# Kernel tuning notes

Measured on AMD Instinct MI355X. Metric: run time of the kernel, lower is better.

Reference implementation:

```python
import jax, jax.numpy as jnp
import numpy as np

# Static configuration (matches init_kwargs / input_specs)
B = 4          # number of point clouds (equal-sized)
NPER = 4096    # points per cloud
RATIO = 0.25
MPER = int(NPER * RATIO)  # sampled centroids per cloud
R = 0.2        # ball-query radius
K = 64         # max_num_neighbors
C = 64         # feature dim


def setup_inputs() -> dict:
    key = jax.random.key(0)
    ks = jax.random.split(key, 6)
    N = B * NPER
    x = jax.random.normal(ks[0], (N, C), dtype=jnp.float32)
    pos = jax.random.uniform(ks[1], (N, 3), dtype=jnp.float32)
    batch = (jnp.arange(N) // NPER).astype(jnp.int64)
    weight = jax.random.normal(ks[2], (N,), dtype=jnp.float32)
    # local_nn = Seq(Lin(67,128), ReLU, Lin(128,256), ReLU)
    W1 = jax.random.normal(ks[3], (C + 3, 128), dtype=jnp.float32) / np.float32(np.sqrt(C + 3))
    b1 = jnp.zeros((128,), dtype=jnp.float32)
    W2 = jax.random.normal(ks[4], (128, 256), dtype=jnp.float32) / np.float32(np.sqrt(128))
    b2 = jnp.zeros((256,), dtype=jnp.float32)
    return {"x": x, "pos": pos, "batch": batch, "weight": weight,
            "W1": W1, "b1": b1, "W2": W2, "b2": b2}


def _fps_single(p):
    """Farthest point sampling on one cloud p:[NPER,3] -> MPER int32 indices.
    Deterministic start at index 0 (torch_geometric uses a random start)."""
    n = p.shape[0]
    def step(carry, _):
        mind, last = carry
        d = jnp.sum((p - p[last]) ** 2, axis=-1)
        mind = jnp.minimum(mind, d)
        nxt = jnp.argmax(mind).astype(jnp.int32)
        return (mind, nxt), last
    init = (jnp.full((n,), jnp.inf, dtype=p.dtype), jnp.int32(0))
    _, idx = jax.lax.scan(step, init, None, length=MPER)
    return idx  # [MPER]


def reference(x, pos, batch, weight, W1, b1, W2, b2):
    pos_b = pos.reshape(B, NPER, 3)
    x_b = x.reshape(B, NPER, C)

    # --- FPS per cloud (vectorized over clouds) ---
    idx = jax.vmap(_fps_single)(pos_b)                      # [B, MPER] local indices

    qpos = jnp.take_along_axis(pos_b, idx[:, :, None], axis=1)  # [B, MPER, 3]

    # --- radius ball query: K nearest within r (fixed-size, batch-respecting) ---
    d2 = jnp.sum((qpos[:, :, None, :] - pos_b[:, None, :, :]) ** 2, axis=-1)  # [B,MPER,NPER]
    neg, nbr = jax.lax.top_k(-d2, K)                        # [B, MPER, K]
    valid = (-neg) <= jnp.float32(R * R)                    # [B, MPER, K]

    # --- gather neighbor features / positions ---
    flat = nbr.reshape(B, MPER * K)
    x_j = jnp.take_along_axis(x_b, flat[:, :, None], axis=1).reshape(B, MPER, K, C)
    pos_j = jnp.take_along_axis(pos_b, flat[:, :, None], axis=1).reshape(B, MPER, K, 3)
    rel = pos_j - qpos[:, :, None, :]                       # [B, MPER, K, 3]

    # --- PointNetConv: local_nn(concat(x_j, rel)) then max aggregation ---
    msg = jnp.concatenate([x_j, rel], axis=-1)              # [B, MPER, K, C+3]
    h = jax.nn.relu(jnp.einsum('bmkc,cd->bmkd', msg, W1) + b1)
    h = jax.nn.relu(jnp.einsum('bmkd,de->bmke', h, W2) + b2)
    h = jnp.where(valid[:, :, :, None], h, -jnp.inf)
    x_out = jnp.max(h, axis=2).reshape(B * MPER, -1)        # [B*MPER, 256]

    # --- gather sampled pos / batch / weight using global indices ---
    idx_g = (idx + (jnp.arange(B, dtype=jnp.int32) * NPER)[:, None]).reshape(-1)
    pos_out = pos[idx_g]
    batch_out = batch[idx_g]
    weight_out = weight[idx_g]
    return x_out, pos_out, batch_out, weight_out
```

## Files before the change

### kernel.cpp

```cpp
#include <hip/hip_runtime.h>

#define NPER 4096
#define MPER 1024
#define KNB 64
#define NB 4

typedef __attribute__((ext_vector_type(8))) short short8_t;
typedef __attribute__((ext_vector_type(4))) float f32x4;
typedef __attribute__((ext_vector_type(2))) float f32x2;

__device__ __forceinline__ unsigned short f2bf(float f) {
  union { float f; unsigned u; } v; v.f = f;
  unsigned r = v.u + 0x7fffu + ((v.u >> 16) & 1u);
  return (unsigned short)(r >> 16);
}

__device__ __forceinline__ f32x2 pk_add(f32x2 a, f32x2 b) {
  f32x2 d; asm("v_pk_add_f32 %0, %1, %2" : "=v"(d) : "v"(a), "v"(b)); return d;
}
__device__ __forceinline__ f32x2 pk_mul(f32x2 a, f32x2 b) {
  f32x2 d; asm("v_pk_mul_f32 %0, %1, %2" : "=v"(d) : "v"(a), "v"(b)); return d;
}

#define DPP_KEY_STEP(ctrl)                                                            \
  {                                                                                   \
    unsigned lo = (unsigned)k, hi = (unsigned)(k >> 32);                              \
    unsigned tlo = (unsigned)__builtin_amdgcn_update_dpp((int)lo, (int)lo, ctrl, 0xF, 0xF, false); \
    unsigned thi = (unsigned)__builtin_amdgcn_update_dpp((int)hi, (int)hi, ctrl, 0xF, 0xF, false); \
    unsigned long long tk = ((unsigned long long)thi << 32) | tlo;                    \
    if (tk > k) k = tk;                                                               \
  }

#define U64MAX(a, b) (((a) > (b)) ? (a) : (b))

__global__ __launch_bounds__(256) void fps_kernel(const float* __restrict__ pos,
                                                  int* __restrict__ idxout) {
  __shared__ float4 p4[NPER];
  __shared__ alignas(16) unsigned long long candk[2][4];
  __shared__ int s_idx[MPER];
  const int b = blockIdx.x, t = threadIdx.x;
  const int wid = t >> 6, lane = t & 63;
  const int base = b * NPER;

  for (int i = t; i < NPER; i += 256) {
    p4[i] = make_float4(pos[(size_t)(base + i) * 3 + 0],
                        pos[(size_t)(base + i) * 3 + 1],
                        pos[(size_t)(base + i) * 3 + 2], 0.f);
  }
  __syncthreads();

  f32x2 pxp[8], pyp[8], pzp[8];
  float mnd[16];
  const int i0 = t * 16;
#pragma unroll
  for (int p = 0; p < 8; ++p) {
    float4 a = p4[i0 + 2 * p];
    float4 c = p4[i0 + 2 * p + 1];
    pxp[p] = (f32x2){a.x, c.x};
    pyp[p] = (f32x2){a.y, c.y};
    pzp[p] = (f32x2){a.z, c.z};
  }
#pragma unroll
  for (int j = 0; j < 16; ++j) mnd[j] = __builtin_inff();

  int last = 0;
  for (int it = 0; it < MPER; ++it) {
    if (t == 0) s_idx[it] = last;
    if (it == MPER - 1) break;
    const float4 q = p4[last];
    const f32x2 nqx = (f32x2){-q.x, -q.x};
    const f32x2 nqy = (f32x2){-q.y, -q.y};
    const f32x2 nqz = (f32x2){-q.z, -q.z};
    float bv = -1.0f; int bj = 0;
#pragma unroll
    for (int p = 0; p < 8; ++p) {
      f32x2 dx = pk_add(pxp[p], nqx);
      f32x2 dy = pk_add(pyp[p], nqy);
      f32x2 dz = pk_add(pzp[p], nqz);
      f32x2 s = pk_add(pk_add(pk_mul(dx, dx), pk_mul(dy, dy)), pk_mul(dz, dz));
      float m0 = fminf(mnd[2 * p], s.x);     mnd[2 * p] = m0;
      if (m0 > bv) { bv = m0; bj = 2 * p; }
      float m1 = fminf(mnd[2 * p + 1], s.y); mnd[2 * p + 1] = m1;
      if (m1 > bv) { bv = m1; bj = 2 * p + 1; }
    }
    const int bi = i0 + bj;
    union { float f; unsigned u; } fu; fu.f = bv;
    unsigned long long k = ((unsigned long long)fu.u << 32) | (0xFFFFFFFFu - (unsigned)bi);
    DPP_KEY_STEP(0x128)
    DPP_KEY_STEP(0x124)
    DPP_KEY_STEP(0x122)
    DPP_KEY_STEP(0x121)
    DPP_KEY_STEP(0x142)
    DPP_KEY_STEP(0x143)
    if (lane == 63) candk[it & 1][wid] = k;
    __syncthreads();
    const ulonglong2* ck = (const ulonglong2*)&candk[it & 1][0];
    ulonglong2 c0 = ck[0], c1 = ck[1];
    unsigned long long m0 = U64MAX(c0.x, c0.y);
    unsigned long long m1 = U64MAX(c1.x, c1.y);
    unsigned long long mg = U64MAX(m0, m1);
    last = (int)(0xFFFFFFFFu - (unsigned)mg);
  }
  __syncthreads();
  for (int i = t; i < MPER; i += 256) idxout[b * MPER + i] = s_idx[i];
}

#define CAP 1024
__global__ __launch_bounds__(256) void ballq_kernel(const float* __restrict__ pos,
                                                    const int* __restrict__ idx,
                                                    int* __restrict__ nbr) {
  __shared__ float cd[CAP];
  __shared__ int   ci[CAP];
  __shared__ int   s_cnt;
  const int c = blockIdx.x;
  const int b = c >> 10;
  const int t = threadIdx.x;
  const int base = b * NPER;
  if (t == 0) s_cnt = 0;
  __syncthreads();
  const int qi = idx[c];
  const float qx = pos[(size_t)(base + qi) * 3 + 0];
  const float qy = pos[(size_t)(base + qi) * 3 + 1];
  const float qz = pos[(size_t)(base + qi) * 3 + 2];
  const float r2f = (float)(0.2 * 0.2);
#pragma unroll
  for (int s = 0; s < 16; ++s) {
    const int i = t + s * 256;
    float dx = __fsub_rn(qx, pos[(size_t)(base + i) * 3 + 0]);
    float dy = __fsub_rn(qy, pos[(size_t)(base + i) * 3 + 1]);
    float dz = __fsub_rn(qz, pos[(size_t)(base + i) * 3 + 2]);
    float d = __fadd_rn(__fadd_rn(__fmul_rn(dx, dx), __fmul_rn(dy, dy)), __fmul_rn(dz, dz));
    if (d <= r2f) {
      int p = atomicAdd(&s_cnt, 1);
      if (p < CAP) { cd[p] = d; ci[p] = i; }
    }
  }
  __syncthreads();
  int n = s_cnt; if (n > CAP) n = CAP;
  if (n > KNB) {
    int P = 64; while (P < n) P <<= 1;
    for (int i = n + t; i < P; i += 256) { cd[i] = __builtin_inff(); ci[i] = 0x7fffffff; }
    __syncthreads();
    for (int k2 = 2; k2 <= P; k2 <<= 1) {
      for (int j = k2 >> 1; j > 0; j >>= 1) {
        for (int i = t; i < P; i += 256) {
          const int ixj = i ^ j;
          if (ixj > i) {
            const bool up = ((i & k2) == 0);
            float a = cd[i], bb = cd[ixj];
            int ia = ci[i], ib = ci[ixj];
            const bool gt = (a > bb) || (a == bb && ia > ib);
            if (gt == up) { cd[i] = bb; cd[ixj] = a; ci[i] = ib; ci[ixj] = ia; }
          }
        }
        __syncthreads();
      }
    }
  }
  if (t < KNB) nbr[c * KNB + t] = (t < n) ? ci[t] : -1;
}

__global__ __launch_bounds__(256) void prep_kernel(const float* __restrict__ W1,
                                                   const float* __restrict__ W2,
                                                   unsigned short* __restrict__ w1f,
                                                   unsigned short* __restrict__ w2f) {
  const int f = blockIdx.x * 256 + threadIdx.x;
  if (f < 12288) {
    const int frag = f >> 9, r = f & 511, lane = r >> 3, e = r & 7;
    const int nt = frag / 3, kt = frag % 3;
    const int n = nt * 16 + (lane & 15);
    const int k = kt * 32 + (lane >> 4) * 8 + e;
    float v = (k < 67) ? W1[k * 128 + n] : 0.f;
    w1f[f] = f2bf(v);
  } else if (f < 12288 + 32768) {
    const int g = f - 12288;
    const int frag = g >> 9, r = g & 511, lane = r >> 3, e = r & 7;
    const int nt = frag >> 2, kt = frag & 3;
    const int n = nt * 16 + (lane & 15);
    const int k = kt * 32 + (lane >> 4) * 8 + e;
    w2f[g] = f2bf(W2[k * 256 + n]);
  }
}

__global__ __launch_bounds__(256) void mlp_kernel(const float* __restrict__ x,
                                                  const float* __restrict__ pos,
                                                  const int* __restrict__ idx,
                                                  const int* __restrict__ nbr,
                                                  const unsigned short* __restrict__ w1f,
                                                  const unsigned short* __restrict__ w2f,
                                                  const float* __restrict__ b1,
                                                  const float* __restrict__ b2,
                                                  float* __restrict__ out) {
  __shared__ alignas(16) unsigned short s_msg[64][104];
  __shared__ alignas(16) unsigned short s_h1[64][136];
  __shared__ int   s_valid[64];
  __shared__ float s_red[4][256];

  const int c = blockIdx.x;
  const int b = c >> 10;
  const int t = threadIdx.x;
  const int wave = t >> 6, lane = t & 63;
  const int base = b * NPER;

  const int qi = idx[c];
  const float q0 = pos[(size_t)(base + qi) * 3 + 0];
  const float q1 = pos[(size_t)(base + qi) * 3 + 1];
  const float q2 = pos[(size_t)(base + qi) * 3 + 2];

  const int nbrv = nbr[c * KNB + lane];
  s_valid[lane] = (nbrv >= 0) ? 1 : 0;

#pragma unroll 4
  for (int i = 0; i < 16; ++i) {
    const int k = wave * 16 + i;
    const int j = __shfl(nbrv, k, 64);
    float f = 0.f;
    if (j >= 0) f = x[(size_t)(base + j) * 64 + lane];
    s_msg[k][lane] = f2bf(f);
    if (lane < 40) {
      float rv = 0.f;
      if (lane < 3 && j >= 0) {
        float p = pos[(size_t)(base + j) * 3 + lane];
        float qq = (lane == 0) ? q0 : ((lane == 1) ? q1 : q2);
        rv = __fsub_rn(p, qq);
      }
      s_msg[k][64 + lane] = f2bf(rv);
    }
  }
  __syncthreads();

  const int row = wave * 16 + (lane & 15);
  const int kofs = (lane >> 4) * 8;

  short8_t a1[3];
#pragma unroll
  for (int kt = 0; kt < 3; ++kt)
    a1[kt] = *(const short8_t*)&s_msg[row][kt * 32 + kofs];
  f32x4 acc1[8];
#pragma unroll
  for (int nt = 0; nt < 8; ++nt) acc1[nt] = (f32x4){0.f, 0.f, 0.f, 0.f};
#pragma unroll
  for (int kt = 0; kt < 3; ++kt) {
#pragma unroll
    for (int nt = 0; nt < 8; ++nt) {
      short8_t bf = *(const short8_t*)&w1f[((nt * 3 + kt) * 64 + lane) * 8];
      acc1[nt] = __builtin_amdgcn_mfma_f32_16x16x32_bf16(a1[kt], bf, acc1[nt], 0, 0, 0);
    }
  }
#pragma unroll
  for (int nt = 0; nt < 8; ++nt) {
    const int n = nt * 16 + (lane & 15);
    const float bias = b1[n];
    f32x4 v = acc1[nt];
#pragma unroll
    for (int e = 0; e < 4; ++e) {
      const int m = wave * 16 + (lane >> 4) * 4 + e;
      float h = v[e] + bias;
      h = (h > 0.f) ? h : 0.f;
      s_h1[m][n] = f2bf(h);
    }
  }
  __syncthreads();

  short8_t a2[4];
#pragma unroll
  for (int kt = 0; kt < 4; ++kt)
    a2[kt] = *(const short8_t*)&s_h1[row][kt * 32 + kofs];
  f32x4 acc2[16];
#pragma unroll
  for (int nt = 0; nt < 16; ++nt) acc2[nt] = (f32x4){0.f, 0.f, 0.f, 0.f};
#pragma unroll
  for (int kt = 0; kt < 4; ++kt) {
#pragma unroll
    for (int nt = 0; nt < 16; ++nt) {
      short8_t bf = *(const short8_t*)&w2f[((nt * 4 + kt) * 64 + lane) * 8];
      acc2[nt] = __builtin_amdgcn_mfma_f32_16x16x32_bf16(a2[kt], bf, acc2[nt], 0, 0, 0);
    }
  }
  const int m0 = wave * 16 + (lane >> 4) * 4;
  const int vld0 = s_valid[m0 + 0], vld1 = s_valid[m0 + 1];
  const int vld2 = s_valid[m0 + 2], vld3 = s_valid[m0 + 3];
#pragma unroll
  for (int nt = 0; nt < 16; ++nt) {
    const int n = nt * 16 + (lane & 15);
    const float bias = b2[n];
    f32x4 d = acc2[nt];
    float best = -__builtin_inff();
    {
      float h;
      h = d[0] + bias; h = (h > 0.f) ? h : 0.f; if (vld0) best = fmaxf(best, h);
      h = d[1] + bias; h = (h > 0.f) ? h : 0.f; if (vld1) best = fmaxf(best, h);
      h = d[2] + bias; h = (h > 0.f) ? h : 0.f; if (vld2) best = fmaxf(best, h);
      h = d[3] + bias; h = (h > 0.f) ? h : 0.f; if (vld3) best = fmaxf(best, h);
    }
    best = fmaxf(best, __shfl_xor(best, 16, 64));
    best = fmaxf(best, __shfl_xor(best, 32, 64));
    if ((lane >> 4) == 0) s_red[wave][n] = best;
  }
  __syncthreads();
  const float r = fmaxf(fmaxf(s_red[0][t], s_red[1][t]), fmaxf(s_red[2][t], s_red[3][t]));
  out[(size_t)c * 256 + t] = r;
}

__global__ __launch_bounds__(256) void tail_kernel(const float* __restrict__ pos,
                                                   const float* __restrict__ weight,
                                                   const int* __restrict__ idx,
                                                   float* __restrict__ out) {
  const int t = blockIdx.x * 256 + threadIdx.x;
  if (t >= NB * MPER) return;
  const int b = t >> 10;
  const int qi = idx[t];
  const int g = b * NPER + qi;
  float* pos_out = out + 1048576;
  float* batch_out = out + 1048576 + 12288;
  float* w_out = out + 1048576 + 12288 + 4096;
  pos_out[t * 3 + 0] = pos[(size_t)g * 3 + 0];
  pos_out[t * 3 + 1] = pos[(size_t)g * 3 + 1];
  pos_out[t * 3 + 2] = pos[(size_t)g * 3 + 2];
  batch_out[t] = (float)b;
  w_out[t] = weight[g];
}

extern "C" void kernel_launch(void* const* d_in, const int* in_sizes, int n_in,
                              void* d_out, int out_size, void* d_ws, size_t ws_size,
                              hipStream_t stream) {
  const float* x      = (const float*)d_in[0];
  const float* pos    = (const float*)d_in[1];
  const float* weight = (const float*)d_in[3];
  const float* W1     = (const float*)d_in[4];
  const float* b1     = (const float*)d_in[5];
  const float* W2     = (const float*)d_in[6];
  const float* b2     = (const float*)d_in[7];
  float* out = (float*)d_out;

  char* ws = (char*)d_ws;
  int* idx = (int*)ws;
  int* nbr = (int*)(ws + 16384);
  unsigned short* w1f = (unsigned short*)(ws + 16384 + 1048576);
  unsigned short* w2f = (unsigned short*)(ws + 16384 + 1048576 + 24576);

  prep_kernel<<<176, 256, 0, stream>>>(W1, W2, w1f, w2f);
  fps_kernel<<<NB, 256, 0, stream>>>(pos, idx);
  ballq_kernel<<<NB * MPER, 256, 0, stream>>>(pos, idx, nbr);
  mlp_kernel<<<NB * MPER, 256, 0, stream>>>(x, pos, idx, nbr, w1f, w2f, b1, b2, out);
  tail_kernel<<<16, 256, 0, stream>>>(pos, weight, idx, out);
}
```

Baseline: 782.8 us.

## Replace FPS barrier with tagged spin-wait and fuse ball query into MLP

The FPS loop drops its per-iteration __syncthreads. Each wave's candidate key now carries a 10-bit iteration tag and is published with a workgroup-scoped atomic store, and every wave spins until all four slots hold the current tag. The ball-query kernel is merged into the MLP kernel, so neighbor indices stay in shared memory and the global nbr round trip and one launch go away. The risks are spin-wait livelock or ordering hazards across the double-buffered slots, and higher LDS use per MLP block, which may reduce occupancy.

```diff
diff --git a/kernel.cpp b/kernel.cpp
--- a/kernel.cpp
+++ b/kernel.cpp
@@ -36,12 +36,13 @@
 __global__ __launch_bounds__(256) void fps_kernel(const float* __restrict__ pos,
                                                   int* __restrict__ idxout) {
   __shared__ float4 p4[NPER];
-  __shared__ alignas(16) unsigned long long candk[2][4];
+  __shared__ unsigned long long candk[2][4];
   __shared__ int s_idx[MPER];
   const int b = blockIdx.x, t = threadIdx.x;
   const int wid = t >> 6, lane = t & 63;
   const int base = b * NPER;
 
+  if (t < 8) ((unsigned long long*)candk)[t] = 1023ull;
   for (int i = t; i < NPER; i += 256) {
     p4[i] = make_float4(pos[(size_t)(base + i) * 3 + 0],
                         pos[(size_t)(base + i) * 3 + 1],
@@ -85,50 +86,97 @@
     }
     const int bi = i0 + bj;
     union { float f; unsigned u; } fu; fu.f = bv;
-    unsigned long long k = ((unsigned long long)fu.u << 32) | (0xFFFFFFFFu - (unsigned)bi);
+    const unsigned tg = (unsigned)it & 1023u;
+    unsigned long long k = ((unsigned long long)fu.u << 32) |
+                           ((unsigned long long)(4095u - (unsigned)bi) << 10) | tg;
     DPP_KEY_STEP(0x128)
     DPP_KEY_STEP(0x124)
     DPP_KEY_STEP(0x122)
     DPP_KEY_STEP(0x121)
     DPP_KEY_STEP(0x142)
     DPP_KEY_STEP(0x143)
-    if (lane == 63) candk[it & 1][wid] = k;
-    __syncthreads();
-    const ulonglong2* ck = (const ulonglong2*)&candk[it & 1][0];
-    ulonglong2 c0 = ck[0], c1 = ck[1];
-    unsigned long long m0 = U64MAX(c0.x, c0.y);
-    unsigned long long m1 = U64MAX(c1.x, c1.y);
-    unsigned long long mg = U64MAX(m0, m1);
-    last = (int)(0xFFFFFFFFu - (unsigned)mg);
+    const int s = it & 1;
+    if (lane == 63)
+      __hip_atomic_store(&candk[s][wid], k, __ATOMIC_RELAXED, __HIP_MEMORY_SCOPE_WORKGROUP);
+    unsigned long long k0, k1, k2, k3;
+    for (;;) {
+      k0 = __hip_atomic_load(&candk[s][0], __ATOMIC_RELAXED, __HIP_MEMORY_SCOPE_WORKGROUP);
+      k1 = __hip_atomic_load(&candk[s][1], __ATOMIC_RELAXED, __HIP_MEMORY_SCOPE_WORKGROUP);
+      k2 = __hip_atomic_load(&candk[s][2], __ATOMIC_RELAXED, __HIP_MEMORY_SCOPE_WORKGROUP);
+      k3 = __hip_atomic_load(&candk[s][3], __ATOMIC_RELAXED, __HIP_MEMORY_SCOPE_WORKGROUP);
+      unsigned m = (((unsigned)k0 & 1023u) ^ tg) | (((unsigned)k1 & 1023u) ^ tg) |
+                   (((unsigned)k2 & 1023u) ^ tg) | (((unsigned)k3 & 1023u) ^ tg);
+      if (m == 0) break;
+    }
+    unsigned long long ma = U64MAX(k0, k1);
+    unsigned long long mb = U64MAX(k2, k3);
+    unsigned long long mg = U64MAX(ma, mb);
+    last = 4095 - (int)((mg >> 10) & 0xFFFu);
   }
   __syncthreads();
   for (int i = t; i < MPER; i += 256) idxout[b * MPER + i] = s_idx[i];
 }
 
+__global__ __launch_bounds__(256) void prep_kernel(const float* __restrict__ W1,
+                                                   const float* __restrict__ W2,
+                                                   unsigned short* __restrict__ w1f,
+                                                   unsigned short* __restrict__ w2f) {
+  const int f = blockIdx.x * 256 + threadIdx.x;
+  if (f < 12288) {
+    const int frag = f >> 9, r = f & 511, lane = r >> 3, e = r & 7;
+    const int nt = frag / 3, kt = frag % 3;
+    const int n = nt * 16 + (lane & 15);
+    const int k = kt * 32 + (lane >> 4) * 8 + e;
+    float v = (k < 67) ? W1[k * 128 + n] : 0.f;
+    w1f[f] = f2bf(v);
+  } else if (f < 12288 + 32768) {
+    const int g = f - 12288;
+    const int frag = g >> 9, r = g & 511, lane = r >> 3, e = r & 7;
+    const int nt = frag >> 2, kt = frag & 3;
+    const int n = nt * 16 + (lane & 15);
+    const int k = kt * 32 + (lane >> 4) * 8 + e;
+    w2f[g] = f2bf(W2[k * 256 + n]);
+  }
+}
+
 #define CAP 1024
-__global__ __launch_bounds__(256) void ballq_kernel(const float* __restrict__ pos,
-                                                    const int* __restrict__ idx,
-                                                    int* __restrict__ nbr) {
+__global__ __launch_bounds__(256) void mlp_kernel(const float* __restrict__ x,
+                                                  const float* __restrict__ pos,
+                                                  const int* __restrict__ idx,
+                                                  const unsigned short* __restrict__ w1f,
+                                                  const unsigned short* __restrict__ w2f,
+                                                  const float* __restrict__ b1,
+                                                  const float* __restrict__ b2,
+                                                  float* __restrict__ out) {
   __shared__ float cd[CAP];
   __shared__ int   ci[CAP];
   __shared__ int   s_cnt;
+  __shared__ alignas(16) unsigned short s_msg[64][104];
+  __shared__ alignas(16) unsigned short s_h1[64][136];
+  __shared__ int   s_valid[64];
+  __shared__ float s_red[4][256];
+
   const int c = blockIdx.x;
   const int b = c >> 10;
   const int t = threadIdx.x;
+  const int wave = t >> 6, lane = t & 63;
   const int base = b * NPER;
+
   if (t == 0) s_cnt = 0;
   __syncthreads();
+
   const int qi = idx[c];
-  const float qx = pos[(size_t)(base + qi) * 3 + 0];
-  const float qy = pos[(size_t)(base + qi) * 3 + 1];
-  const float qz = pos[(size_t)(base + qi) * 3 + 2];
+  const float q0 = pos[(size_t)(base + qi) * 3 + 0];
+  const float q1 = pos[(size_t)(base + qi) * 3 + 1];
+  const float q2 = pos[(size_t)(base + qi) * 3 + 2];
   const float r2f = (float)(0.2 * 0.2);
+
 #pragma unroll
   for (int s = 0; s < 16; ++s) {
     const int i = t + s * 256;
-    float dx = __fsub_rn(qx, pos[(size_t)(base + i) * 3 + 0]);
-    float dy = __fsub_rn(qy, pos[(size_t)(base + i) * 3 + 1]);
-    float dz = __fsub_rn(qz, pos[(size_t)(base + i) * 3 + 2]);
+    float dx = __fsub_rn(q0, pos[(size_t)(base + i) * 3 + 0]);
+    float dy = __fsub_rn(q1, pos[(size_t)(base + i) * 3 + 1]);
+    float dz = __fsub_rn(q2, pos[(size_t)(base + i) * 3 + 2]);
     float d = __fadd_rn(__fadd_rn(__fmul_rn(dx, dx), __fmul_rn(dy, dy)), __fmul_rn(dz, dz));
     if (d <= r2f) {
       int p = atomicAdd(&s_cnt, 1);
@@ -157,58 +205,10 @@
       }
     }
   }
-  if (t < KNB) nbr[c * KNB + t] = (t < n) ? ci[t] : -1;
-}
-
-__global__ __launch_bounds__(256) void prep_kernel(const float* __restrict__ W1,
-                                                   const float* __restrict__ W2,
-                                                   unsigned short* __restrict__ w1f,
-                                                   unsigned short* __restrict__ w2f) {
-  const int f = blockIdx.x * 256 + threadIdx.x;
-  if (f < 12288) {
-    const int frag = f >> 9, r = f & 511, lane = r >> 3, e = r & 7;
-    const int nt = frag / 3, kt = frag % 3;
-    const int n = nt * 16 + (lane & 15);
-    const int k = kt * 32 + (lane >> 4) * 8 + e;
-    float v = (k < 67) ? W1[k * 128 + n] : 0.f;
-    w1f[f] = f2bf(v);
-  } else if (f < 12288 + 32768) {
-    const int g = f - 12288;
-    const int frag = g >> 9, r = g & 511, lane = r >> 3, e = r & 7;
-    const int nt = frag >> 2, kt = frag & 3;
-    const int n = nt * 16 + (lane & 15);
-    const int k = kt * 32 + (lane >> 4) * 8 + e;
-    w2f[g] = f2bf(W2[k * 256 + n]);
-  }
-}
-
-__global__ __launch_bounds__(256) void mlp_kernel(const float* __restrict__ x,
-                                                  const float* __restrict__ pos,
-                                                  const int* __restrict__ idx,
-                                                  const int* __restrict__ nbr,
-                                                  const unsigned short* __restrict__ w1f,
-                                                  const unsigned short* __restrict__ w2f,
-                                                  const float* __restrict__ b1,
-                                                  const float* __restrict__ b2,
-                                                  float* __restrict__ out) {
-  __shared__ alignas(16) unsigned short s_msg[64][104];
-  __shared__ alignas(16) unsigned short s_h1[64][136];
-  __shared__ int   s_valid[64];
-  __shared__ float s_red[4][256];
-
-  const int c = blockIdx.x;
-  const int b = c >> 10;
-  const int t = threadIdx.x;
-  const int wave = t >> 6, lane = t & 63;
-  const int base = b * NPER;
-
-  const int qi = idx[c];
-  const float q0 = pos[(size_t)(base + qi) * 3 + 0];
-  const float q1 = pos[(size_t)(base + qi) * 3 + 1];
-  const float q2 = pos[(size_t)(base + qi) * 3 + 2];
-
-  const int nbrv = nbr[c * KNB + lane];
-  s_valid[lane] = (nbrv >= 0) ? 1 : 0;
+
+  const int nn = (n < KNB) ? n : KNB;
+  const int nbrv = (lane < nn) ? ci[lane] : -1;
+  s_valid[lane] = (lane < nn) ? 1 : 0;
 
 #pragma unroll 4
   for (int i = 0; i < 16; ++i) {
@@ -249,15 +249,15 @@
   }
 #pragma unroll
   for (int nt = 0; nt < 8; ++nt) {
-    const int n = nt * 16 + (lane & 15);
-    const float bias = b1[n];
+    const int n2 = nt * 16 + (lane & 15);
+    const float bias = b1[n2];
     f32x4 v = acc1[nt];
 #pragma unroll
     for (int e = 0; e < 4; ++e) {
       const int m = wave * 16 + (lane >> 4) * 4 + e;
       float h = v[e] + bias;
       h = (h > 0.f) ? h : 0.f;
-      s_h1[m][n] = f2bf(h);
+      s_h1[m][n2] = f2bf(h);
     }
   }
   __syncthreads();
@@ -282,8 +282,8 @@
   const int vld2 = s_valid[m0 + 2], vld3 = s_valid[m0 + 3];
 #pragma unroll
   for (int nt = 0; nt < 16; ++nt) {
-    const int n = nt * 16 + (lane & 15);
-    const float bias = b2[n];
+    const int n2 = nt * 16 + (lane & 15);
+    const float bias = b2[n2];
     f32x4 d = acc2[nt];
     float best = -__builtin_inff();
     {
@@ -295,7 +295,7 @@
     }
     best = fmaxf(best, __shfl_xor(best, 16, 64));
     best = fmaxf(best, __shfl_xor(best, 32, 64));
-    if ((lane >> 4) == 0) s_red[wave][n] = best;
+    if ((lane >> 4) == 0) s_red[wave][n2] = best;
   }
   __syncthreads();
   const float r = fmaxf(fmaxf(s_red[0][t], s_red[1][t]), fmaxf(s_red[2][t], s_red[3][t]));
@@ -335,13 +335,11 @@
 
   char* ws = (char*)d_ws;
   int* idx = (int*)ws;
-  int* nbr = (int*)(ws + 16384);
   unsigned short* w1f = (unsigned short*)(ws + 16384 + 1048576);
   unsigned short* w2f = (unsigned short*)(ws + 16384 + 1048576 + 24576);
 
   prep_kernel<<<176, 256, 0, stream>>>(W1, W2, w1f, w2f);
   fps_kernel<<<NB, 256, 0, stream>>>(pos, idx);
-  ballq_kernel<<<NB * MPER, 256, 0, stream>>>(pos, idx, nbr);
-  mlp_kernel<<<NB * MPER, 256, 0, stream>>>(x, pos, idx, nbr, w1f, w2f, b1, b2, out);
+  mlp_kernel<<<NB * MPER, 256, 0, stream>>>(x, pos, idx, w1f, w2f, b1, b2, out);
   tail_kernel<<<16, 256, 0, stream>>>(pos, weight, idx, out);
 }
```

Result: slower. 884.2 us (+13.0%).
